# Performance work log

Measured on AMD Instinct MI355X. Metric: run time of the kernel, lower is better.

The kernel has to match this reference:

```python
import jax, jax.numpy as jnp
import numpy as np

N_NODES = 200000
N_GRAPHS = 2000
D = 128


def setup_inputs() -> dict:
    key = jax.random.key(0)
    ks = jax.random.split(key, 12)
    s = 0.05  # small init scale for numerical stability
    return {
        "node_scalar": jax.random.normal(ks[0], (N_NODES, D), jnp.float32),
        "batch": jnp.sort(jax.random.randint(ks[1], (N_NODES,), 0, N_GRAPHS, jnp.int32)),
        "spin": jax.random.uniform(ks[2], (N_GRAPHS, 1), jnp.float32) * 3.0,
        "Wq": jax.random.normal(ks[3], (D, D), jnp.float32) * s,
        "bq": jax.random.normal(ks[4], (D,), jnp.float32) * s,
        "Wk": jax.random.normal(ks[5], (D, 1), jnp.float32) * s,
        "Wv": jax.random.normal(ks[6], (D, 1), jnp.float32) * s,
        "W1": jax.random.normal(ks[7], (D, D), jnp.float32) * s,
        "b1": jax.random.normal(ks[8], (D,), jnp.float32) * s,
        "W2": jax.random.normal(ks[9], (D, D), jnp.float32) * s,
        "b2": jax.random.normal(ks[10], (D,), jnp.float32) * s,
    }


def reference(node_scalar, batch, spin, Wq, bq, Wk, Wv, W1, b1, W2, b2):
    n_graphs = spin.shape[0]
    d = node_scalar.shape[-1]
    scale = 1.0 / float(np.sqrt(d))

    spin_norm = jnp.maximum(spin, jnp.ones_like(spin))
    q = node_scalar @ Wq.T + bq                    # [N, D]
    k = ((spin / spin_norm) @ Wk.T)[batch]         # [G, D] -> gather -> [N, D]
    v = (spin @ Wv.T)[batch]                       # [G, D] -> gather -> [N, D]

    dot = jnp.sum(q * k, axis=-1, keepdims=True)   # [N, 1]
    attn = jax.nn.softplus(dot * scale)            # [N, 1]
    attn_sum = jax.ops.segment_sum(attn, batch, num_segments=n_graphs)[batch]  # [N, 1]

    x = attn * v / attn_sum                        # [N, D]
    # ResidualLayer(n_layers=2): two act->linear blocks with a residual add
    h = jax.nn.silu(x @ W1.T + b1)
    h = jax.nn.silu(h @ W2.T + b2)
    spin_embed = x + h

    return node_scalar + spin_embed
```

## Files before the change

### kernel.cpp

```cpp
#include <hip/hip_runtime.h>
#include <hip/hip_bf16.h>

typedef unsigned short u16;
typedef __attribute__((ext_vector_type(8))) short short8;
typedef __attribute__((ext_vector_type(4))) float f32x4;

__device__ __forceinline__ float silu_f(float x) { return x / (1.0f + __expf(-x)); }
__device__ __forceinline__ float softplus_f(float x) {
    return (x > 20.0f) ? x : log1pf(__expf(x));
}

__global__ __launch_bounds__(256) void prep_kernel(
    const float* __restrict__ Wq, const float* __restrict__ bq,
    const float* __restrict__ Wk, const float* __restrict__ Wv,
    const float* __restrict__ W1, const float* __restrict__ W2,
    float* __restrict__ wqk, float* __restrict__ u1, float* __restrict__ bqk,
    u16* __restrict__ W2bf, float* __restrict__ asum, int G)
{
    const int tid = threadIdx.x;
    const int bid = blockIdx.x;
    if (bid == 0) {
        __shared__ float sm[128];
        if (tid < 128) {
            float acc = 0.f;
            #pragma unroll 8
            for (int i = 0; i < 128; ++i) acc += Wq[i * 128 + tid] * Wk[i];
            wqk[tid] = acc;
            sm[tid] = bq[tid] * Wk[tid];
        } else {
            const int j = tid - 128;
            float acc = 0.f;
            #pragma unroll 8
            for (int i = 0; i < 128; ++i) acc += W1[j * 128 + i] * Wv[i];
            u1[j] = acc;
        }
        __syncthreads();
        if (tid == 0) {
            float s = 0.f;
            for (int i = 0; i < 128; ++i) s += sm[i];
            bqk[0] = s;
        }
    } else if (bid <= 16) {
        const int base = (bid - 1) * 1024 + tid * 4;
        const float4 w = *reinterpret_cast<const float4*>(W2 + base);
        const float f[4] = {w.x, w.y, w.z, w.w};
        u16 o[4];
        #pragma unroll
        for (int e = 0; e < 4; ++e) {
            __hip_bfloat16 hb = __float2bfloat16(f[e]);
            __builtin_memcpy(&o[e], &hb, 2);
        }
        *reinterpret_cast<ushort4*>(W2bf + base) = make_ushort4(o[0], o[1], o[2], o[3]);
    } else {
        const int i = (bid - 17) * 256 + tid;
        if (i < G) asum[i] = 0.f;
    }
}

__global__ __launch_bounds__(256) void attn_kernel(
    const float* __restrict__ ns, const int* __restrict__ batch,
    const float* __restrict__ spin, const float* __restrict__ wqk,
    const float* __restrict__ bqk, float* __restrict__ attn,
    float* __restrict__ asum, int N)
{
    __shared__ float sattn[128];
    __shared__ int   sbatch[128];
    const int tid = threadIdx.x;
    const int l32 = tid & 31;
    const int hw  = tid >> 5;
    const int rbase = blockIdx.x * 128 + hw * 16;

    const float4 wv = *reinterpret_cast<const float4*>(wqk + l32 * 4);
    const float bq0 = bqk[0];

    #pragma unroll 8
    for (int k = 0; k < 16; ++k) {
        const int n = rbase + k;
        float p = 0.f;
        if (n < N) {
            const float4 x = *reinterpret_cast<const float4*>(ns + (size_t)n * 128 + l32 * 4);
            p = x.x * wv.x + x.y * wv.y + x.z * wv.z + x.w * wv.w;
        }
        #pragma unroll
        for (int off = 16; off > 0; off >>= 1) p += __shfl_xor(p, off, 64);
        if (l32 == 0) {
            float a = 0.f;
            int g = -1;
            if (n < N) {
                g = batch[n];
                const float sp = spin[g];
                const float ratio = sp / fmaxf(sp, 1.0f);
                const float xx = (p + bq0) * ratio * 0.08838834764831845f;
                a = softplus_f(xx);
                attn[n] = a;
            }
            sattn[hw * 16 + k]  = a;
            sbatch[hw * 16 + k] = g;
        }
    }
    __syncthreads();

    if (tid < 128) {
        const int g = sbatch[tid];
        if (g >= 0 && (tid == 0 || sbatch[tid - 1] != g)) {
            float s = 0.f;
            int j = tid;
            while (j < 128 && sbatch[j] == g) { s += sattn[j]; ++j; }
            atomicAdd(&asum[g], s);
        }
    }
}

__global__ __launch_bounds__(256) void main_kernel(
    const float* __restrict__ ns, const int* __restrict__ batch,
    const float* __restrict__ spin, const float* __restrict__ Wv,
    const float* __restrict__ b1, const float* __restrict__ b2,
    const float* __restrict__ u1, const float* __restrict__ attn,
    const float* __restrict__ asum, const u16* __restrict__ W2bf,
    float* __restrict__ out, int N)
{
    __shared__ float c_lds[64];
    __shared__ __align__(16) u16 h1[64][136];
    const int tid = threadIdx.x;
    const int n0 = blockIdx.x * 64;

    if (tid < 64) {
        const int n = n0 + tid;
        float c = 0.f;
        if (n < N) {
            const int g = batch[n];
            c = attn[n] * spin[g] / asum[g];
        }
        c_lds[tid] = c;
    }
    __syncthreads();

    {
        const int j0 = (tid & 31) * 4;
        const int nb = (tid >> 5) * 8;
        const float4 u1v = *reinterpret_cast<const float4*>(u1 + j0);
        const float4 b1v = *reinterpret_cast<const float4*>(b1 + j0);
        const float uu[4] = {u1v.x, u1v.y, u1v.z, u1v.w};
        const float bb[4] = {b1v.x, b1v.y, b1v.z, b1v.w};
        #pragma unroll
        for (int e = 0; e < 8; ++e) {
            const int node = nb + e;
            const float c = c_lds[node];
            u16 pk[4];
            #pragma unroll
            for (int q = 0; q < 4; ++q) {
                const float hv = silu_f(c * uu[q] + bb[q]);
                __hip_bfloat16 hb = __float2bfloat16(hv);
                __builtin_memcpy(&pk[q], &hb, 2);
            }
            *reinterpret_cast<ushort4*>(&h1[node][j0]) =
                make_ushort4(pk[0], pk[1], pk[2], pk[3]);
        }
    }
    __syncthreads();

    const int lane = tid & 63;
    const int w = tid >> 6;
    const int r16 = lane & 15;
    const int g4 = lane >> 4;
    const int nw0 = w * 16;

    short8 a[4];
    const u16* arow = &h1[nw0 + r16][g4 * 8];
    #pragma unroll
    for (int kt = 0; kt < 4; ++kt)
        a[kt] = *reinterpret_cast<const short8*>(arow + kt * 32);

    #pragma unroll
    for (int ct = 0; ct < 8; ++ct) {
        const int i = ct * 16 + r16;
        const u16* brow = W2bf + i * 128 + g4 * 8;
        f32x4 acc = {0.f, 0.f, 0.f, 0.f};
        #pragma unroll
        for (int kt = 0; kt < 4; ++kt) {
            const short8 b = *reinterpret_cast<const short8*>(brow + kt * 32);
            acc = __builtin_amdgcn_mfma_f32_16x16x32_bf16(a[kt], b, acc, 0, 0, 0);
        }
        const float b2i = b2[i];
        const float wvi = Wv[i];
        #pragma unroll
        for (int r = 0; r < 4; ++r) {
            const int nl = nw0 + g4 * 4 + r;
            const int n = n0 + nl;
            if (n < N) {
                const float h2v = silu_f(acc[r] + b2i);
                out[(size_t)n * 128 + i] = ns[(size_t)n * 128 + i] + c_lds[nl] * wvi + h2v;
            }
        }
    }
}

extern "C" void kernel_launch(void* const* d_in, const int* in_sizes, int n_in,
                              void* d_out, int out_size, void* d_ws, size_t ws_size,
                              hipStream_t stream) {
    (void)n_in; (void)out_size; (void)ws_size;
    const float* ns    = (const float*)d_in[0];
    const int*   batch = (const int*)d_in[1];
    const float* spin  = (const float*)d_in[2];
    const float* Wq    = (const float*)d_in[3];
    const float* bq    = (const float*)d_in[4];
    const float* Wk    = (const float*)d_in[5];
    const float* Wv    = (const float*)d_in[6];
    const float* W1    = (const float*)d_in[7];
    const float* b1    = (const float*)d_in[8];
    const float* W2    = (const float*)d_in[9];
    const float* b2    = (const float*)d_in[10];
    float* out = (float*)d_out;

    const int N = in_sizes[0] / 128;
    const int G = in_sizes[2];

    float* ws = (float*)d_ws;
    size_t o = 0;
    float* asum = ws + o; o += (size_t)((G + 63) & ~63);
    float* attn = ws + o; o += (size_t)((N + 63) & ~63);
    float* wqk  = ws + o; o += 128;
    float* u1   = ws + o; o += 128;
    float* bqk  = ws + o; o += 64;
    u16*   W2bf = (u16*)(ws + o);

    const int zeroBlocks = (G + 255) / 256;
    prep_kernel<<<dim3(17 + zeroBlocks), dim3(256), 0, stream>>>(
        Wq, bq, Wk, Wv, W1, W2, wqk, u1, bqk, W2bf, asum, G);
    attn_kernel<<<dim3((N + 127) / 128), dim3(256), 0, stream>>>(
        ns, batch, spin, wqk, bqk, attn, asum, N);
    main_kernel<<<dim3((N + 63) / 64), dim3(256), 0, stream>>>(
        ns, batch, spin, Wv, b1, b2, u1, attn, asum, W2bf, out, N);
}
```

Before: 295.6 us.

## Stage output epilogue through LDS for coalesced stores; LDS segment-sum in attn

The main kernel now writes the per-node MLP result into a shared-memory tile that reuses the h1 buffer. It then does the residual add with node_scalar as row-contiguous float4 loads and stores, replacing the scattered per-lane 4-byte accesses strided by row. The attention kernel replaces the serial per-segment scan with shared-memory atomics into slots indexed relative to the block's first graph id, followed by one global atomic per non-empty slot. The slot indexing assumes fewer than 128 distinct graph ids span each 128-node block. That holds for sorted batch ids without large gaps.

Measured after the change: 274.6 us. -7.1%, faster.

```diff
diff --git a/kernel.cpp b/kernel.cpp
--- a/kernel.cpp
+++ b/kernel.cpp
@@ -65,6 +65,7 @@
 {
     __shared__ float sattn[128];
     __shared__ int   sbatch[128];
+    __shared__ float slots[128];
     const int tid = threadIdx.x;
     const int l32 = tid & 31;
     const int hw  = tid >> 5;
@@ -72,6 +73,7 @@
 
     const float4 wv = *reinterpret_cast<const float4*>(wqk + l32 * 4);
     const float bq0 = bqk[0];
+    if (tid < 128) slots[tid] = 0.f;
 
     #pragma unroll 8
     for (int k = 0; k < 16; ++k) {
@@ -100,14 +102,15 @@
     }
     __syncthreads();
 
+    const int g0 = sbatch[0];
     if (tid < 128) {
         const int g = sbatch[tid];
-        if (g >= 0 && (tid == 0 || sbatch[tid - 1] != g)) {
-            float s = 0.f;
-            int j = tid;
-            while (j < 128 && sbatch[j] == g) { s += sattn[j]; ++j; }
-            atomicAdd(&asum[g], s);
-        }
+        if (g >= 0) atomicAdd(&slots[g - g0], sattn[tid]);
+    }
+    __syncthreads();
+    if (tid < 128) {
+        const float s = slots[tid];
+        if (s != 0.f) atomicAdd(&asum[g0 + tid], s);
     }
 }
 
@@ -120,7 +123,9 @@
     float* __restrict__ out, int N)
 {
     __shared__ float c_lds[64];
-    __shared__ __align__(16) u16 h1[64][136];
+    __shared__ __align__(16) unsigned char smem[64 * 132 * 4];
+    u16   (*h1)[136]   = reinterpret_cast<u16(*)[136]>(smem);
+    float (*hout)[132] = reinterpret_cast<float(*)[132]>(smem);
     const int tid = threadIdx.x;
     const int n0 = blockIdx.x * 64;
 
@@ -170,6 +175,10 @@
     #pragma unroll
     for (int kt = 0; kt < 4; ++kt)
         a[kt] = *reinterpret_cast<const short8*>(arow + kt * 32);
+    __syncthreads();
+
+    const float c_mine[4] = { c_lds[nw0 + g4 * 4 + 0], c_lds[nw0 + g4 * 4 + 1],
+                              c_lds[nw0 + g4 * 4 + 2], c_lds[nw0 + g4 * 4 + 3] };
 
     #pragma unroll
     for (int ct = 0; ct < 8; ++ct) {
@@ -186,11 +195,24 @@
         #pragma unroll
         for (int r = 0; r < 4; ++r) {
             const int nl = nw0 + g4 * 4 + r;
-            const int n = n0 + nl;
-            if (n < N) {
-                const float h2v = silu_f(acc[r] + b2i);
-                out[(size_t)n * 128 + i] = ns[(size_t)n * 128 + i] + c_lds[nl] * wvi + h2v;
-            }
+            hout[nl][i] = c_mine[r] * wvi + silu_f(acc[r] + b2i);
+        }
+    }
+    __syncthreads();
+
+    #pragma unroll
+    for (int e = 0; e < 8; ++e) {
+        const int flat = e * 1024 + tid * 4;
+        const int row = flat >> 7;
+        const int col = flat & 127;
+        const int n = n0 + row;
+        if (n < N) {
+            const float4 hv = *reinterpret_cast<const float4*>(&hout[row][col]);
+            const float4 nv = *reinterpret_cast<const float4*>(ns + (size_t)n * 128 + col);
+            float4 ov;
+            ov.x = nv.x + hv.x; ov.y = nv.y + hv.y;
+            ov.z = nv.z + hv.z; ov.w = nv.w + hv.w;
+            *reinterpret_cast<float4*>(out + (size_t)n * 128 + col) = ov;
         }
     }
 }
```
